# Optimization experiments

Measured on AMD Instinct MI355X. Metric: run time of the kernel, lower is better.

The kernel has to match this reference:

```python
import jax, jax.numpy as jnp
import numpy as np

NEG_INF = jnp.float32(-1e30)
EPS = 1e-7  # keras.backend.ctc_batch_cost epsilon


def ctc_batch_cost(y_true, y_pred):
    """Faithful CTC loss (keras ctc_batch_cost semantics): y_pred are
    probabilities [B,T,C], blank = C-1, full input/label lengths.
    Returns per-example negative log likelihood [B,1]."""
    B, T, C = y_pred.shape
    L = y_true.shape[1]
    S = 2 * L + 1  # extended label length (blanks interleaved)
    blank = C - 1

    log_probs = jnp.log(y_pred + EPS)  # [B,T,C]

    # Extended label sequence: blank, l0, blank, l1, ..., blank  -> [B,S]
    ext = jnp.full((B, S), blank, dtype=y_true.dtype)
    ext = ext.at[:, 1::2].set(y_true)

    # Skip transition allowed at s if ext[s] != blank and ext[s] != ext[s-2]
    skip = jnp.concatenate(
        [jnp.zeros((B, 2), dtype=bool),
         (ext[:, 2:] != blank) & (ext[:, 2:] != ext[:, :-2])], axis=1)  # [B,S]

    # Gather log-probs of extended labels per timestep: [T,B,S]
    lp_ext = jnp.take_along_axis(log_probs, ext[:, None, :], axis=2)  # [B,T,S]
    lp_ext = jnp.transpose(lp_ext, (1, 0, 2))  # [T,B,S]

    # alpha init at t=0: only positions 0 (blank) and 1 (first label)
    alpha0 = jnp.full((B, S), NEG_INF, dtype=log_probs.dtype)
    alpha0 = alpha0.at[:, 0].set(lp_ext[0, :, 0])
    alpha0 = alpha0.at[:, 1].set(lp_ext[0, :, 1])

    pad1 = jnp.full((B, 1), NEG_INF, dtype=log_probs.dtype)
    pad2 = jnp.full((B, 2), NEG_INF, dtype=log_probs.dtype)

    def step(alpha, lp_t):
        a_stay = alpha
        a_prev = jnp.concatenate([pad1, alpha[:, :-1]], axis=1)
        a_skip = jnp.where(skip, jnp.concatenate([pad2, alpha[:, :-2]], axis=1), NEG_INF)
        m = jnp.maximum(jnp.maximum(a_stay, a_prev), a_skip)
        lse = m + jnp.log(jnp.exp(a_stay - m) + jnp.exp(a_prev - m) + jnp.exp(a_skip - m))
        return lse + lp_t, None

    alpha_T, _ = jax.lax.scan(step, alpha0, lp_ext[1:])  # [B,S]

    # log P = logsumexp over last blank and last label positions
    end = jnp.stack([alpha_T[:, S - 1], alpha_T[:, S - 2]], axis=1)  # [B,2]
    loglik = jax.nn.logsumexp(end, axis=1)  # [B]
    return -loglik[:, None]  # [B,1] like keras ctc_batch_cost


def setup_inputs() -> dict:
    key = jax.random.key(0)
    k1, k2 = jax.random.split(key)
    B, T, C, L = 512, 512, 128, 32
    y_true = jax.random.randint(k1, (B, L), 0, C - 1, dtype=jnp.int64 if jax.config.read('jax_enable_x64') else jnp.int32)
    y_pred = jax.random.uniform(k2, (B, T, C), dtype=jnp.float32)
    return {"y_true": y_true, "y_pred": y_pred}


def reference(y_true, y_pred):
    return ctc_batch_cost(y_true, y_pred)
```

## Files before the change

kernel.cpp:

```cpp
#include <hip/hip_runtime.h>


#define EPSF 1e-7f

constexpr int T_  = 512;
constexpr int C_  = 128;
constexpr int L_  = 32;
constexpr int NG  = 127;
constexpr int PFG = 4;
constexpr int NLD = 17;

__launch_bounds__(64)
__global__ void ctc_loss_kernel(const int* __restrict__ y_true,
                                const float* __restrict__ y_pred,
                                float* __restrict__ out) {
    const int b    = blockIdx.x;
    const int lane = threadIdx.x;

    const float* bb  = y_pred + (size_t)b * T_ * C_;
    const int*   lbl = y_true + b * L_;

    int   cls[7];
    float sg[7];
#pragma unroll
    for (int i = 0; i < 7; ++i) {
        const int v = lane - i;
        int   c = C_ - 1;
        float s = 0.f;
        if (v >= 1 && (v & 1)) {
            c = lbl[(v - 1) >> 1];
            if (v >= 3 && c != lbl[((v - 1) >> 1) - 1]) s = 1.f;
        }
        cls[i] = c;
        sg[i]  = s;
    }
    float msk[9];
#pragma unroll
    for (int i = 0; i < 9; ++i) msk[i] = (lane >= i) ? 1.f : 0.f;

    float a       = (lane < 2) ? (bb[cls[0]] + EPSF) : 0.f;
    float a64     = 0.f;
    int   e_total = 0;

    float Q[PFG][NLD];
    auto loadq = [&](float (&Qk)[NLD], const float* __restrict__ r) {
        Qk[0]  = r[cls[0]];          Qk[1]  = r[cls[1]];
        Qk[2]  = r[cls[2]];          Qk[3]  = r[cls[3]];
        Qk[4]  = r[cls[4]];          Qk[5]  = r[cls[5]];
        Qk[6]  = r[cls[6]];
        Qk[7]  = r[C_ + cls[0]];     Qk[8]  = r[C_ + cls[1]];
        Qk[9]  = r[C_ + cls[2]];     Qk[10] = r[C_ + cls[3]];
        Qk[11] = r[C_ + cls[4]];
        Qk[12] = r[2 * C_ + cls[0]]; Qk[13] = r[2 * C_ + cls[1]];
        Qk[14] = r[2 * C_ + cls[2]];
        Qk[15] = r[3 * C_ + cls[0]]; Qk[16] = r[3 * C_ + cls[1]];
    };
#pragma unroll
    for (int k = 0; k < PFG; ++k) loadq(Q[k], bb + (size_t)(1 + 4 * k) * C_);

    float smp[16];
    auto sample = [&]() {
#pragma unroll
        for (int i = 0; i < 16; ++i) smp[i] = __shfl(a, 4 * i + 3);
    };
    sample();

    auto group4 = [&](float (&Qk)[NLD]) {
        float A[9];
        A[0] = a;
#pragma unroll
        for (int i = 1; i <= 8; ++i) A[i] = __shfl_up(a, i) * msk[i];

        float B[7];
#pragma unroll
        for (int i = 0; i <= 6; ++i)
            B[i] = (A[i] + A[i + 1] + sg[i] * A[i + 2]) * (Qk[i] + EPSF);
        float Cc[5];
#pragma unroll
        for (int i = 0; i <= 4; ++i)
            Cc[i] = (B[i] + B[i + 1] + sg[i] * B[i + 2]) * (Qk[7 + i] + EPSF);
        float D[3];
#pragma unroll
        for (int i = 0; i <= 2; ++i)
            D[i] = (Cc[i] + Cc[i + 1] + sg[i] * Cc[i + 2]) * (Qk[12 + i] + EPSF);

        float z = a64;
        z = (z + A[0])  * (Qk[1]  + EPSF);
        z = (z + B[0])  * (Qk[8]  + EPSF);
        z = (z + Cc[0]) * (Qk[13] + EPSF);
        z = (z + D[0])  * (Qk[16] + EPSF);
        a64 = z;

        a = (D[0] + D[1] + sg[0] * D[2]) * (Qk[15] + EPSF);
    };

    auto apply_scale = [&]() {
        float t[8];
#pragma unroll
        for (int i = 0; i < 8; ++i) t[i] = fmaxf(smp[i], smp[i + 8]);
#pragma unroll
        for (int i = 0; i < 4; ++i) t[i] = fmaxf(t[i], t[i + 4]);
        float m = fmaxf(fmaxf(t[0], t[1]), fmaxf(t[2], t[3]));
        m = fmaxf(m, 1e-30f);
        const unsigned eb = __float_as_uint(m) >> 23;
        e_total += (int)eb - 127;
        const float inv = __uint_as_float((254u - eb) << 23);
        a *= inv;
        a64 *= inv;
    };

    for (int g0 = 0; g0 < 124; g0 += PFG) {
#pragma unroll
        for (int k = 0; k < PFG; ++k) {
            const int g = g0 + k;
            group4(Q[k]);
            apply_scale();
            sample();
            const int gn = g + PFG;
            if (gn < NG) loadq(Q[k], bb + (size_t)(1 + 4 * gn) * C_);
        }
    }

    float qo[3], qb[3];
#pragma unroll
    for (int r = 0; r < 3; ++r) {
        const float* rp = bb + (size_t)(509 + r) * C_;
        qo[r] = rp[cls[0]];
        qb[r] = rp[cls[1]];
    }

    group4(Q[0]); apply_scale(); sample();
    group4(Q[1]); apply_scale(); sample();
    group4(Q[2]); apply_scale();

#pragma unroll
    for (int r = 0; r < 3; ++r) {
        float prev = __shfl_up(a, 1) * msk[1];
        float sk   = __shfl_up(a, 2) * msk[2];
        const float anew = (a + prev + sg[0] * sk) * (qo[r] + EPSF);
        a64 = (a64 + a) * (qb[r] + EPSF);
        a = anew;
    }

    if (lane == 63) {
        out[b] = -(__logf(a + a64) + (float)e_total * 0.6931471805599453f);
    }
}

extern "C" void kernel_launch(void* const* d_in, const int* in_sizes, int n_in,
                              void* d_out, int out_size, void* d_ws, size_t ws_size,
                              hipStream_t stream) {
    const int*   y_true = (const int*)d_in[0];
    const float* y_pred = (const float*)d_in[1];
    float*       out    = (float*)d_out;

    const int B = out_size;
    ctc_loss_kernel<<<B, 64, 0, stream>>>(y_true, y_pred, out);
}
```

Measured before the change: 225.1 us.

## Stream timestep rows into LDS ring buffer via async global_load_lds

Replaces the register-held 4-deep prefetch of gathered per-row probabilities with a 16-slot LDS ring buffer. Each group's 4 rows are loaded with asynchronous global-to-LDS loads about 15 groups ahead, gated by explicit vmcnt waits. The per-lane gathers then come from LDS. This is meant to hide global memory latency behind the serial recurrence. It adds LDS traffic and relies on hand-counted vmcnt values being correct.

```diff
diff --git a/kernel.cpp b/kernel.cpp
--- a/kernel.cpp
+++ b/kernel.cpp
@@ -3,17 +3,28 @@
 
 #define EPSF 1e-7f
 
-constexpr int T_  = 512;
-constexpr int C_  = 128;
-constexpr int L_  = 32;
-constexpr int NG  = 127;
-constexpr int PFG = 4;
-constexpr int NLD = 17;
+constexpr int T_   = 512;
+constexpr int C_   = 128;
+constexpr int L_   = 32;
+constexpr int NG   = 127;
+constexpr int NLD  = 17;
+constexpr int NBUF = 16;
+
+static_assert(NG == 127, "");
+
+__device__ __forceinline__ void gl16(const float* gp, float* lp) {
+    __builtin_amdgcn_global_load_lds(
+        (const __attribute__((address_space(1))) void*)gp,
+        (__attribute__((address_space(3))) void*)lp,
+        16, 0, 0);
+}
 
 __launch_bounds__(64)
 __global__ void ctc_loss_kernel(const int* __restrict__ y_true,
                                 const float* __restrict__ y_pred,
                                 float* __restrict__ out) {
+    __shared__ float smem[NBUF * 512];
+
     const int b    = blockIdx.x;
     const int lane = threadIdx.x;
 
@@ -42,8 +53,15 @@
     float a64     = 0.f;
     int   e_total = 0;
 
-    float Q[PFG][NLD];
-    auto loadq = [&](float (&Qk)[NLD], const float* __restrict__ r) {
+    auto issueG = [&](int g) {
+        const float* src = bb + (size_t)(1 + 4 * g) * C_ + lane * 4;
+        float* dst = &smem[(g & (NBUF - 1)) * 512];
+        gl16(src,       dst);
+        gl16(src + 256, dst + 256);
+    };
+
+    auto ldsq = [&](float (&Qk)[NLD], int g) {
+        const float* r = &smem[(g & (NBUF - 1)) * 512];
         Qk[0]  = r[cls[0]];          Qk[1]  = r[cls[1]];
         Qk[2]  = r[cls[2]];          Qk[3]  = r[cls[3]];
         Qk[4]  = r[cls[4]];          Qk[5]  = r[cls[5]];
@@ -55,15 +73,12 @@
         Qk[14] = r[2 * C_ + cls[2]];
         Qk[15] = r[3 * C_ + cls[0]]; Qk[16] = r[3 * C_ + cls[1]];
     };
-#pragma unroll
-    for (int k = 0; k < PFG; ++k) loadq(Q[k], bb + (size_t)(1 + 4 * k) * C_);
 
     float smp[16];
     auto sample = [&]() {
 #pragma unroll
         for (int i = 0; i < 16; ++i) smp[i] = __shfl(a, 4 * i + 3);
     };
-    sample();
 
     auto group4 = [&](float (&Qk)[NLD]) {
         float A[9];
@@ -109,36 +124,60 @@
         a64 *= inv;
     };
 
-    for (int g0 = 0; g0 < 124; g0 += PFG) {
+    sample();
+
 #pragma unroll
-        for (int k = 0; k < PFG; ++k) {
-            const int g = g0 + k;
-            group4(Q[k]);
-            apply_scale();
-            sample();
-            const int gn = g + PFG;
-            if (gn < NG) loadq(Q[k], bb + (size_t)(1 + 4 * gn) * C_);
-        }
+    for (int k = 0; k < 15; ++k) issueG(k);
+    asm volatile("s_waitcnt vmcnt(28)" ::: "memory");
+
+    float QA[NLD], QB[NLD];
+    ldsq(QA, 0);
+
+    for (int g0 = 0; g0 < 112; g0 += 2) {
+        issueG(g0 + 15);
+        asm volatile("s_waitcnt vmcnt(28)" ::: "memory");
+        ldsq(QB, g0 + 1);
+        group4(QA);
+        apply_scale();
+        sample();
+
+        issueG(g0 + 16);
+        asm volatile("s_waitcnt vmcnt(28)" ::: "memory");
+        ldsq(QA, g0 + 2);
+        group4(QB);
+        apply_scale();
+        sample();
     }
 
-    float qo[3], qb[3];
+    float qo[3], qb2[3];
 #pragma unroll
     for (int r = 0; r < 3; ++r) {
         const float* rp = bb + (size_t)(509 + r) * C_;
-        qo[r] = rp[cls[0]];
-        qb[r] = rp[cls[1]];
+        qo[r]  = rp[cls[0]];
+        qb2[r] = rp[cls[1]];
     }
 
-    group4(Q[0]); apply_scale(); sample();
-    group4(Q[1]); apply_scale(); sample();
-    group4(Q[2]); apply_scale();
+    asm volatile("s_waitcnt vmcnt(0)" ::: "memory");
+
+    for (int g0 = 112; g0 < 126; g0 += 2) {
+        ldsq(QB, g0 + 1);
+        group4(QA);
+        apply_scale();
+        sample();
+        ldsq(QA, g0 + 2);
+        group4(QB);
+        apply_scale();
+        sample();
+    }
+    group4(QA);
+    apply_scale();
 
 #pragma unroll
     for (int r = 0; r < 3; ++r) {
         float prev = __shfl_up(a, 1) * msk[1];
         float sk   = __shfl_up(a, 2) * msk[2];
         const float anew = (a + prev + sg[0] * sk) * (qo[r] + EPSF);
-        a64 = (a64 + a) * (qb[r] + EPSF);
+        a64 = (a64 + a) * (qb2[r] + EPSF);
         a = anew;
     }
 
```

Result: slower. 231.9 us (+3.0%).
